# Optimization experiments

Hardware: AMD Instinct MI355X
Metric: run time of the kernel (lower is better)

The kernel has to match this reference:

```python
import jax, jax.numpy as jnp
import numpy as np


def setup_inputs() -> dict:
    key = jax.random.key(0)
    ks = jax.random.split(key, 12)
    B, S, D, HS, O = 512, 128, 128, 256, 1
    stdv = 1.0 / np.sqrt(HS)
    u = lambda k, shp: jax.random.uniform(k, shp, jnp.float32, -stdv, stdv)
    return {
        "H": jax.random.normal(ks[0], (B, S, D), jnp.float32),
        "y0": jax.random.normal(ks[1], (B, O), jnp.float32),
        "Wa": u(ks[2], (D, S)),
        "Ua": u(ks[3], (HS, S)),
        "ba": u(ks[4], (S,)),
        "Va": u(ks[5], (S, S)),
        "W": u(ks[6], (D, 4 * HS)),
        "U": u(ks[7], (HS, 4 * HS)),
        "bias": u(ks[8], (4 * HS,)),
        "Wy": u(ks[9], (O, 4 * HS)),
        "fc_W": u(ks[10], (O, HS)),
        "fc_b": u(ks[11], (O,)),
    }


def reference(H, y0, Wa, Ua, ba, Va, W, U, bias, Wy, fc_W, fc_b):
    B, S, D = H.shape
    HS = U.shape[0]
    # s_t in the original is initialized to zeros and never updated, so the
    # s_t @ Ua term is a constant zero; kept explicitly for faithfulness.
    s0 = jnp.zeros((B, HS), H.dtype)
    sUa = s0 @ Ua  # [B, S], zeros
    h0 = jnp.zeros((B, HS), H.dtype)
    c0 = jnp.zeros((B, HS), H.dtype)

    def step(carry, h_t):  # h_t: [B, D] = H[:, t, :]
        h_prev, c_prev, y_prev = carry
        logits = jnp.tanh(h_t @ Wa + sUa + ba) @ Va          # [B, S]
        beta = jax.nn.softmax(logits, axis=1)                # [B, S]
        pooled = jnp.einsum('bs,bsd->bd', beta, H)           # attention pool over full seq
        gates = pooled @ W + h_prev @ U + y_prev @ Wy + bias # [B, 4*HS]
        i_t, f_t, g_t, o_t = jnp.split(gates, 4, axis=1)
        c_new = jax.nn.sigmoid(f_t) * c_prev + jax.nn.sigmoid(i_t) * jnp.tanh(g_t)
        h_new = jax.nn.sigmoid(o_t) * jnp.tanh(c_new)
        y_new = h_new @ fc_W.T + fc_b                        # [B, O]
        return (h_new, c_new, y_new), h_new

    xs = jnp.transpose(H, (1, 0, 2))  # [S, B, D]
    (h_f, c_f, y_f), seq = jax.lax.scan(step, (h0, c0, y0), xs)
    hidden_seq = jnp.transpose(seq, (1, 0, 2))  # [B, S, HS]
    return y_f, hidden_seq
```

## Files before the change

kernel.cpp:

```cpp
#include <hip/hip_runtime.h>
#include <hip/hip_bf16.h>


using bf16x8 = __attribute__((ext_vector_type(8))) short;
using f32x4  = __attribute__((ext_vector_type(4))) float;
using f32x2  = __attribute__((ext_vector_type(2))) float;
using u16x4  = __attribute__((ext_vector_type(4))) unsigned short;

#define DEV static __device__ __forceinline__

DEV unsigned short f2bf(float x) {
    unsigned u = __float_as_uint(x);
    u += 0x7fffu + ((u >> 16) & 1u);
    return (unsigned short)(u >> 16);
}
DEV float bf2f(unsigned short s) { return __uint_as_float(((unsigned)s) << 16); }
DEV float sigm(float x) { return 1.0f / (1.0f + __expf(-x)); }
DEV float tanh_f(float x) { float e = __expf(2.0f * x); return 1.0f - 2.0f / (e + 1.0f); }
DEV f32x4 mfma16(bf16x8 a, bf16x8 b, f32x4 c) {
    return __builtin_amdgcn_mfma_f32_16x16x32_bf16(a, b, c, 0, 0, 0);
}

DEV void stage128(const unsigned short* __restrict__ src, unsigned short* dst, int rows, int tid) {
    int chunks = rows * 16;
    for (int i = tid; i < chunks; i += 256) {
        int r = i >> 4, c = (i & 15) << 3;
        *(bf16x8*)(dst + r * 136 + c) = *(const bf16x8*)(src + r * 128 + c);
    }
}
DEV void stage128f(const float* __restrict__ src, unsigned short* dst, int rows, int tid) {
    int chunks = rows * 16;
    for (int i = tid; i < chunks; i += 256) {
        int r = i >> 4, c = (i & 15) << 3;
        const float* s = src + r * 128 + c;
        bf16x8 o;
        #pragma unroll
        for (int e = 0; e < 8; ++e) o[e] = (short)f2bf(s[e]);
        *(bf16x8*)(dst + r * 136 + c) = o;
    }
}

__global__ void k_prepw(const float* __restrict__ Wa, const float* __restrict__ Va,
                        const float* __restrict__ W, const float* __restrict__ U,
                        const float* __restrict__ fcW, const float* __restrict__ Wy,
                        unsigned short* __restrict__ WaT, unsigned short* __restrict__ VaT,
                        unsigned short* __restrict__ WT, unsigned short* __restrict__ Upk) {
    int idx = blockIdx.x * 256 + threadIdx.x;
    if (idx < 16384) {
        int n = idx >> 7, k = idx & 127;
        WaT[idx] = f2bf(Wa[k * 128 + n]);
    } else if (idx < 32768) {
        int i = idx - 16384;
        int n = i >> 7, k = i & 127;
        VaT[i] = f2bf(Va[k * 128 + n]);
    } else if (idx < 163840) {
        int i = idx - 32768;
        int n = i >> 7, k = i & 127;
        WT[i] = f2bf(W[k * 1024 + n]);
    } else if (idx < 425984) {
        int i = idx - 163840;
        int j = i & 7, ll = (i >> 3) & 63, tt = (i >> 9) & 7, kc = (i >> 12) & 7, w = i >> 15;
        int k = kc * 32 + (ll >> 4) * 8 + j;
        int n = (tt >> 1) * 256 + w * 32 + (tt & 1) * 16 + (ll & 15);
        Upk[i] = f2bf(U[k * 1024 + n] + fcW[k] * Wy[n]);
    }
}

__global__ __launch_bounds__(256) void k_prept(const float* __restrict__ H,
                                               unsigned short* __restrict__ HT) {
    __shared__ unsigned short tl[128 * 130];
    int b = blockIdx.x, tid = threadIdx.x;
    const float* Hb = H + (size_t)b * 16384;
    for (int i = tid; i < 16384; i += 256) {
        int s = i >> 7, d = i & 127;
        tl[s * 130 + d] = f2bf(Hb[i]);
    }
    __syncthreads();
    unsigned short* HTb = HT + (size_t)b * 16384;
    for (int i = tid; i < 16384; i += 256) {
        int d = i >> 7, s = i & 127;
        HTb[i] = tl[s * 130 + d];
    }
}

__global__ __launch_bounds__(256) void k_att(const float* __restrict__ H,
                                             const unsigned short* __restrict__ WaT,
                                             const unsigned short* __restrict__ VaT,
                                             const unsigned short* __restrict__ HT,
                                             const float* __restrict__ ba,
                                             unsigned short* __restrict__ poolT) {
    __shared__ unsigned short A1[128 * 136];
    __shared__ unsigned short B1[128 * 136];
    int tid = threadIdx.x, b = blockIdx.x;
    int w = tid >> 6, l = tid & 63, q = l >> 4, r = l & 15;

    stage128f(H + (size_t)b * 16384, A1, 128, tid);
    stage128(WaT, B1, 128, tid);
    __syncthreads();
    f32x4 acc[2][8] = {};
    #pragma unroll
    for (int kc = 0; kc < 4; ++kc)
        #pragma unroll
        for (int mt = 0; mt < 2; ++mt) {
            bf16x8 a = *(const bf16x8*)(A1 + (w * 32 + mt * 16 + r) * 136 + kc * 32 + q * 8);
            #pragma unroll
            for (int nt = 0; nt < 8; ++nt) {
                bf16x8 bb = *(const bf16x8*)(B1 + (nt * 16 + r) * 136 + kc * 32 + q * 8);
                acc[mt][nt] = mfma16(a, bb, acc[mt][nt]);
            }
        }
    __syncthreads();
    #pragma unroll
    for (int nt = 0; nt < 8; ++nt) {
        float bav = ba[nt * 16 + r];
        #pragma unroll
        for (int mt = 0; mt < 2; ++mt)
            #pragma unroll
            for (int j = 0; j < 4; ++j)
                B1[(w * 32 + mt * 16 + q * 4 + j) * 136 + nt * 16 + r] =
                    f2bf(tanh_f(acc[mt][nt][j] + bav));
    }
    stage128(VaT, A1, 128, tid);
    __syncthreads();

    f32x4 lacc[2][8] = {};
    #pragma unroll
    for (int kc = 0; kc < 4; ++kc)
        #pragma unroll
        for (int mt = 0; mt < 2; ++mt) {
            bf16x8 a = *(const bf16x8*)(B1 + (w * 32 + mt * 16 + r) * 136 + kc * 32 + q * 8);
            #pragma unroll
            for (int nt = 0; nt < 8; ++nt) {
                bf16x8 bb = *(const bf16x8*)(A1 + (nt * 16 + r) * 136 + kc * 32 + q * 8);
                lacc[mt][nt] = mfma16(a, bb, lacc[mt][nt]);
            }
        }
    float inv_[2][4];
    #pragma unroll
    for (int mt = 0; mt < 2; ++mt)
        #pragma unroll
        for (int j = 0; j < 4; ++j) {
            float mx = lacc[mt][0][j];
            #pragma unroll
            for (int nt = 1; nt < 8; ++nt) mx = fmaxf(mx, lacc[mt][nt][j]);
            mx = fmaxf(mx, __shfl_xor(mx, 1));
            mx = fmaxf(mx, __shfl_xor(mx, 2));
            mx = fmaxf(mx, __shfl_xor(mx, 4));
            mx = fmaxf(mx, __shfl_xor(mx, 8));
            float s = 0.f;
            #pragma unroll
            for (int nt = 0; nt < 8; ++nt) {
                float e = __expf(lacc[mt][nt][j] - mx);
                lacc[mt][nt][j] = e;
                s += e;
            }
            s += __shfl_xor(s, 1);
            s += __shfl_xor(s, 2);
            s += __shfl_xor(s, 4);
            s += __shfl_xor(s, 8);
            inv_[mt][j] = 1.0f / s;
        }
    __syncthreads();
    #pragma unroll
    for (int mt = 0; mt < 2; ++mt)
        #pragma unroll
        for (int nt = 0; nt < 8; ++nt)
            #pragma unroll
            for (int j = 0; j < 4; ++j)
                B1[(w * 32 + mt * 16 + q * 4 + j) * 136 + nt * 16 + r] =
                    f2bf(lacc[mt][nt][j] * inv_[mt][j]);
    stage128(HT + (size_t)b * 16384, A1, 128, tid);
    __syncthreads();

    f32x4 pacc[2][8] = {};
    #pragma unroll
    for (int kc = 0; kc < 4; ++kc)
        #pragma unroll
        for (int mt = 0; mt < 2; ++mt) {
            bf16x8 a = *(const bf16x8*)(B1 + (w * 32 + mt * 16 + r) * 136 + kc * 32 + q * 8);
            #pragma unroll
            for (int nt = 0; nt < 8; ++nt) {
                bf16x8 bb = *(const bf16x8*)(A1 + (nt * 16 + r) * 136 + kc * 32 + q * 8);
                pacc[mt][nt] = mfma16(a, bb, pacc[mt][nt]);
            }
        }
    unsigned short* pb = poolT + (size_t)b * 16384;
    #pragma unroll
    for (int mt = 0; mt < 2; ++mt)
        #pragma unroll
        for (int nt = 0; nt < 8; ++nt)
            #pragma unroll
            for (int j = 0; j < 4; ++j)
                pb[(w * 32 + mt * 16 + q * 4 + j) * 128 + nt * 16 + r] = f2bf(pacc[mt][nt][j]);
}

__global__ __launch_bounds__(256) void k_gx(const unsigned short* __restrict__ poolT,
                                            const unsigned short* __restrict__ WT,
                                            const float* __restrict__ bias,
                                            const float* __restrict__ Wy,
                                            const float* __restrict__ y0,
                                            const float* __restrict__ fcb,
                                            unsigned short* __restrict__ Gxp) {
    __shared__ unsigned short a_lds[64 * 136];
    __shared__ unsigned short b_lds[128 * 136];
    int tid = threadIdx.x;
    int mblk = blockIdx.x >> 3, nb = blockIdx.x & 7;
    int b = mblk >> 1, t0 = (mblk & 1) * 64, n0 = nb * 128;
    stage128(poolT + (size_t)b * 16384 + t0 * 128, a_lds, 64, tid);
    stage128(WT + (size_t)n0 * 128, b_lds, 128, tid);
    __syncthreads();
    int w = tid >> 6, l = tid & 63, q = l >> 4, r = l & 15;
    f32x4 acc[8] = {};
    #pragma unroll
    for (int kc = 0; kc < 4; ++kc) {
        bf16x8 a = *(const bf16x8*)(a_lds + (w * 16 + r) * 136 + kc * 32 + q * 8);
        #pragma unroll
        for (int nt = 0; nt < 8; ++nt) {
            bf16x8 bb = *(const bf16x8*)(b_lds + (nt * 16 + r) * 136 + kc * 32 + q * 8);
            acc[nt] = mfma16(a, bb, acc[nt]);
        }
    }
    int g = b >> 1, rowbit = b & 1;
    float fcb0 = fcb[0];
    float y00 = y0[b];
    #pragma unroll
    for (int nt = 0; nt < 8; ++nt) {
        int col = n0 + nt * 16 + r;
        float bv = bias[col], wv = Wy[col];
        int c = col & 255;
        int w_s = c >> 5, ch = (c >> 4) & 1, r_s = c & 15;
        int gate = col >> 8;
        int l_s = (ch * 2 + rowbit) * 16 + r_s;
        size_t base = ((((size_t)g * 128) * 8 + w_s) * 64 + l_s) * 4 + gate;
        #pragma unroll
        for (int j = 0; j < 4; ++j) {
            int t = t0 + w * 16 + q * 4 + j;
            float yb = (t == 0) ? y00 : fcb0;
            Gxp[base + (size_t)t * 2048] = f2bf(acc[nt][j] + bv + yb * wv);
        }
    }
}

__global__ __launch_bounds__(512, 2) void k_seq(const unsigned short* __restrict__ Gxp,
                                                const unsigned short* __restrict__ Upk,
                                                const float* __restrict__ fcW,
                                                const float* __restrict__ fcb,
                                                float* __restrict__ out) {
    extern __shared__ __align__(16) char dynbuf[];
    unsigned short* u2   = (unsigned short*)dynbuf;
    unsigned short* h_fl = (unsigned short*)(dynbuf + 131072);
    float* scr           = (float*)(dynbuf + 134144);
    float* ypart         = (float*)(dynbuf + 143360);

    int tid = threadIdx.x;
    int g = blockIdx.x;
    int w = tid >> 6, l = tid & 63, q = l >> 4, r = l & 15;
    int row = q & 1, ch = q >> 1;
    int rr = (r < 2) ? r : 2;
    float fc_b0 = fcb[0];

    bf16x8 u_res[5][8];
    {
        const bf16x8* up = (const bf16x8*)Upk;
        const int kcs[5] = {0, 1, 2, 5, 6};
        #pragma unroll
        for (int i = 0; i < 5; ++i)
            #pragma unroll
            for (int tt = 0; tt < 8; ++tt)
                u_res[i][tt] = up[((w * 8 + kcs[i]) * 8 + tt) * 64 + l];
    }
    #pragma unroll
    for (int kcL = 0; kcL < 2; ++kcL)
        #pragma unroll
        for (int tt = 0; tt < 8; ++tt) {
            size_t gofs = (size_t)(((w * 8 + 3 + kcL) * 8 + tt) * 64 + l) * 8;
            size_t lofs = (size_t)(((w * 2 + kcL) * 8 + tt) * 64 + l) * 8;
            *(bf16x8*)(u2 + lofs) = *(const bf16x8*)(Upk + gofs);
        }

    float fw0 = fcW[w * 32 + ch * 16 + r];
    float c_st = 0.f, hv_st = 0.f;

    for (int i = tid; i < 1536; i += 512) h_fl[i] = 0;
    __syncthreads();

    const unsigned short* gxp = Gxp + ((((size_t)g * 128 * 8 + w) * 64 + l) * 4);
    const bf16x8* u7p = (const bf16x8*)Upk + (w * 8 + 7) * 512 + l;
    float* outp = out + 512 + (size_t)(g * 2 + row) * 32768 + w * 32 + ch * 16 + r;
    float* scw = scr + (w * 16 + r) * 18;
    const float* scrd = scw + 2 * ch + row;

    for (int t = 0; t < 128; ++t) {
        unsigned short* hp = h_fl + (t & 1) * 768;
        unsigned short* hn = h_fl + ((t & 1) ^ 1) * 768;

        if (t > 0) {
            *outp = hv_st;
            outp += 256;
        }

        bf16x8 u7[8];
        #pragma unroll
        for (int tt = 0; tt < 8; ++tt) u7[tt] = u7p[tt * 64];

        u16x4 gxv = *(const u16x4*)gxp;

        f32x4 acc[8] = {};
        #pragma unroll
        for (int i = 0; i < 3; ++i) {
            bf16x8 a = *(const bf16x8*)(hp + ((i * 4 + q) * 3 + rr) * 8);
            #pragma unroll
            for (int tt = 0; tt < 8; ++tt) acc[tt] = mfma16(a, u_res[i][tt], acc[tt]);
        }
        #pragma unroll
        for (int kcL = 0; kcL < 2; ++kcL) {
            bf16x8 a = *(const bf16x8*)(hp + (((3 + kcL) * 4 + q) * 3 + rr) * 8);
            #pragma unroll
            for (int tt = 0; tt < 8; ++tt) {
                bf16x8 u = *(const bf16x8*)(u2 + (size_t)(((w * 2 + kcL) * 8 + tt) * 64 + l) * 8);
                acc[tt] = mfma16(a, u, acc[tt]);
            }
        }
        #pragma unroll
        for (int i = 0; i < 2; ++i) {
            bf16x8 a = *(const bf16x8*)(hp + (((5 + i) * 4 + q) * 3 + rr) * 8);
            #pragma unroll
            for (int tt = 0; tt < 8; ++tt) acc[tt] = mfma16(a, u_res[3 + i][tt], acc[tt]);
        }
        {
            bf16x8 a = *(const bf16x8*)(hp + ((7 * 4 + q) * 3 + rr) * 8);
            #pragma unroll
            for (int tt = 0; tt < 8; ++tt) acc[tt] = mfma16(a, u7[tt], acc[tt]);
        }

        if (q == 0) {
            #pragma unroll
            for (int tt = 0; tt < 8; ++tt)
                *(f32x2*)(scw + tt * 2) = f32x2{acc[tt][0], acc[tt][1]};
        }
        asm volatile("s_waitcnt lgkmcnt(0)" ::: "memory");
        __builtin_amdgcn_sched_barrier(0);
        float av[4];
        #pragma unroll
        for (int gp = 0; gp < 4; ++gp) av[gp] = scrd[gp * 4];

        {
            float iv = sigm(av[0] + bf2f(gxv[0]));
            float fv = sigm(av[1] + bf2f(gxv[1]));
            float gv = tanh_f(av[2] + bf2f(gxv[2]));
            float ov = sigm(av[3] + bf2f(gxv[3]));
            float c = fv * c_st + iv * gv;
            c_st = c;
            float hv = ov * tanh_f(c);
            hn[((w * 4 + ch * 2 + (r >> 3)) * 3 + row) * 8 + (r & 7)] = f2bf(hv);
            hv_st = hv;
            if (t == 127) {
                float v = hv * fw0;
                v += __shfl_xor(v, 1);
                v += __shfl_xor(v, 2);
                v += __shfl_xor(v, 4);
                v += __shfl_xor(v, 8);
                v += __shfl_xor(v, 32);
                if (r == 0 && ch == 0) ypart[w * 2 + row] = v;
            }
        }
        gxp += 2048;
        asm volatile("s_waitcnt lgkmcnt(0)\n\ts_barrier" ::: "memory");
    }

    *outp = hv_st;

    __syncthreads();
    if (tid < 2) {
        float y = fc_b0;
        #pragma unroll
        for (int ww = 0; ww < 8; ++ww) y += ypart[ww * 2 + tid];
        out[g * 2 + tid] = y;
    }
}

extern "C" void kernel_launch(void* const* d_in, const int* in_sizes, int n_in,
                              void* d_out, int out_size, void* d_ws, size_t ws_size,
                              hipStream_t stream) {
    const float* H    = (const float*)d_in[0];
    const float* y0   = (const float*)d_in[1];
    const float* Wa   = (const float*)d_in[2];
    const float* ba   = (const float*)d_in[4];
    const float* Va   = (const float*)d_in[5];
    const float* W    = (const float*)d_in[6];
    const float* U    = (const float*)d_in[7];
    const float* bias = (const float*)d_in[8];
    const float* Wy   = (const float*)d_in[9];
    const float* fcW  = (const float*)d_in[10];
    const float* fcb  = (const float*)d_in[11];
    float* out = (float*)d_out;
    char* ws = (char*)d_ws;

    unsigned short* HT    = (unsigned short*)(ws);
    unsigned short* poolT = (unsigned short*)(ws + 16777216);
    unsigned short* Gxp   = (unsigned short*)(ws + 2 * 16777216);
    unsigned short* WaT   = (unsigned short*)(ws + 2 * 16777216 + 134217728);
    unsigned short* VaT   = WaT + 16384;
    unsigned short* WT    = VaT + 16384;
    unsigned short* Upk   = WT + 131072;

    hipFuncSetAttribute((const void*)k_seq, hipFuncAttributeMaxDynamicSharedMemorySize, 143424);

    hipLaunchKernelGGL(k_prepw, dim3(1664), dim3(256), 0, stream, Wa, Va, W, U, fcW, Wy,
                       WaT, VaT, WT, Upk);
    hipLaunchKernelGGL(k_prept, dim3(512), dim3(256), 0, stream, H, HT);
    hipLaunchKernelGGL(k_att, dim3(512), dim3(256), 0, stream, H, WaT, VaT, HT, ba, poolT);
    hipLaunchKernelGGL(k_gx, dim3(8192), dim3(256), 0, stream, poolT, WT, bias, Wy, y0, fcb, Gxp);
    hipLaunchKernelGGL(k_seq, dim3(256), dim3(512), 143424, stream, Gxp, Upk, fcW, fcb, out);
}
```

Measured before the change: 575.9 us.

## Keep all of U register-resident except LDS chunk; repack Gx for vector loads

```diff
diff --git a/kernel.cpp b/kernel.cpp
--- a/kernel.cpp
+++ b/kernel.cpp
@@ -5,7 +5,6 @@
 using bf16x8 = __attribute__((ext_vector_type(8))) short;
 using f32x4  = __attribute__((ext_vector_type(4))) float;
 using f32x2  = __attribute__((ext_vector_type(2))) float;
-using u16x4  = __attribute__((ext_vector_type(4))) unsigned short;
 
 #define DEV static __device__ __forceinline__
 
@@ -204,10 +203,13 @@
     __shared__ unsigned short a_lds[64 * 136];
     __shared__ unsigned short b_lds[128 * 136];
     int tid = threadIdx.x;
-    int mblk = blockIdx.x >> 3, nb = blockIdx.x & 7;
-    int b = mblk >> 1, t0 = (mblk & 1) * 64, n0 = nb * 128;
-    stage128(poolT + (size_t)b * 16384 + t0 * 128, a_lds, 64, tid);
-    stage128(WT + (size_t)n0 * 128, b_lds, 128, tid);
+    int b = blockIdx.x >> 4;
+    int thalf = (blockIdx.x >> 3) & 1;
+    int ws = blockIdx.x & 7;
+    stage128(poolT + (size_t)b * 16384 + thalf * 64 * 128, a_lds, 64, tid);
+    #pragma unroll
+    for (int gate = 0; gate < 4; ++gate)
+        stage128(WT + (size_t)(gate * 256 + ws * 32) * 128, b_lds + gate * 32 * 136, 32, tid);
     __syncthreads();
     int w = tid >> 6, l = tid & 63, q = l >> 4, r = l & 15;
     f32x4 acc[8] = {};
@@ -220,32 +222,34 @@
             acc[nt] = mfma16(a, bb, acc[nt]);
         }
     }
-    int g = b >> 1, rowbit = b & 1;
-    float fcb0 = fcb[0];
-    float y00 = y0[b];
+    int g = b >> 1, jb = b & 1;
+    float fcb0 = fcb[0], y00 = y0[b];
+    float bv[8], wv[8];
     #pragma unroll
     for (int nt = 0; nt < 8; ++nt) {
-        int col = n0 + nt * 16 + r;
-        float bv = bias[col], wv = Wy[col];
-        int c = col & 255;
-        int w_s = c >> 5, ch = (c >> 4) & 1, r_s = c & 15;
-        int gate = col >> 8;
-        int l_s = (ch * 2 + rowbit) * 16 + r_s;
-        size_t base = ((((size_t)g * 128) * 8 + w_s) * 64 + l_s) * 4 + gate;
-        #pragma unroll
-        for (int j = 0; j < 4; ++j) {
-            int t = t0 + w * 16 + q * 4 + j;
-            float yb = (t == 0) ? y00 : fcb0;
-            Gxp[base + (size_t)t * 2048] = f2bf(acc[nt][j] + bv + yb * wv);
-        }
-    }
-}
-
-__global__ __launch_bounds__(512, 2) void k_seq(const unsigned short* __restrict__ Gxp,
-                                                const unsigned short* __restrict__ Upk,
-                                                const float* __restrict__ fcW,
-                                                const float* __restrict__ fcb,
-                                                float* __restrict__ out) {
+        int col = (nt >> 1) * 256 + ws * 32 + (nt & 1) * 16 + r;
+        bv[nt] = bias[col];
+        wv[nt] = Wy[col];
+    }
+    #pragma unroll
+    for (int j = 0; j < 4; ++j) {
+        int t = thalf * 64 + w * 16 + q * 4 + j;
+        float yb = (t == 0) ? y00 : fcb0;
+        bf16x8 o;
+        #pragma unroll
+        for (int nt = 0; nt < 8; ++nt)
+            o[nt] = (short)f2bf(acc[nt][j] + bv[nt] + yb * wv[nt]);
+        size_t addr = ((((size_t)g * 128 + t) * 8 + ws) * 16 + r) * 16 + jb * 8;
+        *(bf16x8*)(Gxp + addr) = o;
+    }
+}
+
+__attribute__((amdgpu_waves_per_eu(2, 2)))
+__global__ __launch_bounds__(512) void k_seq(const unsigned short* __restrict__ Gxp,
+                                             const unsigned short* __restrict__ Upk,
+                                             const float* __restrict__ fcW,
+                                             const float* __restrict__ fcb,
+                                             float* __restrict__ out) {
     extern __shared__ __align__(16) char dynbuf[];
     unsigned short* u2   = (unsigned short*)dynbuf;
     unsigned short* h_fl = (unsigned short*)(dynbuf + 131072);
@@ -259,12 +263,12 @@
     int rr = (r < 2) ? r : 2;
     float fc_b0 = fcb[0];
 
-    bf16x8 u_res[5][8];
+    bf16x8 u_res[6][8];
     {
         const bf16x8* up = (const bf16x8*)Upk;
-        const int kcs[5] = {0, 1, 2, 5, 6};
-        #pragma unroll
-        for (int i = 0; i < 5; ++i)
+        const int kcs[6] = {0, 1, 2, 5, 6, 7};
+        #pragma unroll
+        for (int i = 0; i < 6; ++i)
             #pragma unroll
             for (int tt = 0; tt < 8; ++tt)
                 u_res[i][tt] = up[((w * 8 + kcs[i]) * 8 + tt) * 64 + l];
@@ -284,8 +288,7 @@
     for (int i = tid; i < 1536; i += 512) h_fl[i] = 0;
     __syncthreads();
 
-    const unsigned short* gxp = Gxp + ((((size_t)g * 128 * 8 + w) * 64 + l) * 4);
-    const bf16x8* u7p = (const bf16x8*)Upk + (w * 8 + 7) * 512 + l;
+    const unsigned short* gxq = Gxp + (size_t)g * 262144 + w * 256 + r * 16;
     float* outp = out + 512 + (size_t)(g * 2 + row) * 32768 + w * 32 + ch * 16 + r;
     float* scw = scr + (w * 16 + r) * 18;
     const float* scrd = scw + 2 * ch + row;
@@ -299,11 +302,11 @@
             outp += 256;
         }
 
-        bf16x8 u7[8];
-        #pragma unroll
-        for (int tt = 0; tt < 8; ++tt) u7[tt] = u7p[tt * 64];
-
-        u16x4 gxv = *(const u16x4*)gxp;
+        bf16x8 gxa, gxb;
+        if (q == 0) {
+            gxa = *(const bf16x8*)gxq;
+            gxb = *(const bf16x8*)(gxq + 8);
+        }
 
         f32x4 acc[8] = {};
         #pragma unroll
@@ -322,15 +325,18 @@
             }
         }
         #pragma unroll
-        for (int i = 0; i < 2; ++i) {
+        for (int i = 0; i < 3; ++i) {
             bf16x8 a = *(const bf16x8*)(hp + (((5 + i) * 4 + q) * 3 + rr) * 8);
             #pragma unroll
             for (int tt = 0; tt < 8; ++tt) acc[tt] = mfma16(a, u_res[3 + i][tt], acc[tt]);
         }
-        {
-            bf16x8 a = *(const bf16x8*)(hp + ((7 * 4 + q) * 3 + rr) * 8);
-            #pragma unroll
-            for (int tt = 0; tt < 8; ++tt) acc[tt] = mfma16(a, u7[tt], acc[tt]);
+
+        if (q == 0) {
+            #pragma unroll
+            for (int tt = 0; tt < 8; ++tt) {
+                acc[tt][0] += bf2f((unsigned short)gxa[tt]);
+                acc[tt][1] += bf2f((unsigned short)gxb[tt]);
+            }
         }
 
         if (q == 0) {
@@ -345,10 +351,10 @@
         for (int gp = 0; gp < 4; ++gp) av[gp] = scrd[gp * 4];
 
         {
-            float iv = sigm(av[0] + bf2f(gxv[0]));
-            float fv = sigm(av[1] + bf2f(gxv[1]));
-            float gv = tanh_f(av[2] + bf2f(gxv[2]));
-            float ov = sigm(av[3] + bf2f(gxv[3]));
+            float iv = sigm(av[0]);
+            float fv = sigm(av[1]);
+            float gv = tanh_f(av[2]);
+            float ov = sigm(av[3]);
             float c = fv * c_st + iv * gv;
             c_st = c;
             float hv = ov * tanh_f(c);
@@ -364,7 +370,7 @@
                 if (r == 0 && ch == 0) ypart[w * 2 + row] = v;
             }
         }
-        gxp += 2048;
+        gxq += 2048;
         asm volatile("s_waitcnt lgkmcnt(0)\n\ts_barrier" ::: "memory");
     }
 
```

Measured after the change: 573.1 us. No clear change (-0.5%).
